# Optimization experiments

Measured on AMD Instinct MI355X. Metric: run time of the kernel, lower is better.

## Reference

```python
import jax, jax.numpy as jnp
import numpy as np

NS, NP, EJ, ER = 10000, 2048, 32768, 32768  # skills, job/resume pairs, edges
D, H = 1536, 8
NEG_SLOPE_ATT = 0.2   # GAT attention leaky_relu
NEG_SLOPE = 0.01      # F.leaky_relu / nn.LeakyReLU default


def setup_inputs() -> dict:
    key = jax.random.key(0)
    ks = jax.random.split(key, 20)
    rn = lambda k, shp, s=1.0: jax.random.normal(k, shp, dtype=jnp.float32) * s
    s_d = 1.0 / np.sqrt(D)
    return {
        "x_skill": rn(ks[0], (NS, D)),
        "x_job": rn(ks[1], (NP, D)),
        "x_resume": rn(ks[2], (NP, D)),
        # GraphConv params (lin_rel has bias, lin_root bias=False in PyG)
        "W_rel": rn(ks[3], (D, D), s_d),
        "b_rel": jnp.zeros((D,), jnp.float32),
        "W_root": rn(ks[4], (D, D), s_d),
        # GATConv params (heads=8, concat=False)
        "W_gat_src": rn(ks[5], (D, H * D), s_d),
        "W_gat_dst": rn(ks[6], (D, H * D), s_d),
        "att_src": rn(ks[7], (H, D), s_d),
        "att_dst": rn(ks[8], (H, D), s_d),
        "b_gat": jnp.zeros((D,), jnp.float32),
        # MLP: [3072 -> 512 -> 128 -> 1]
        "W1": rn(ks[9], (2 * D, 512), 1.0 / np.sqrt(2 * D)),
        "b1": jnp.zeros((512,), jnp.float32),
        "W2": rn(ks[10], (512, 128), 1.0 / np.sqrt(512)),
        "b2": jnp.zeros((128,), jnp.float32),
        "W3": rn(ks[11], (128, 1), 1.0 / np.sqrt(128)),
        "b3": jnp.zeros((1,), jnp.float32),
        # edge lists (src = skill idx, dst = job/resume idx)
        "edge_src_job": jax.random.randint(ks[12], (EJ,), 0, NS, dtype=jnp.int32),
        "edge_dst_job": jax.random.randint(ks[13], (EJ,), 0, NP, dtype=jnp.int32),
        "edge_src_res": jax.random.randint(ks[14], (ER,), 0, NS, dtype=jnp.int32),
        "edge_dst_res": jax.random.randint(ks[15], (ER,), 0, NP, dtype=jnp.int32),
    }


def reference(x_skill, x_job, x_resume, W_rel, b_rel, W_root,
              W_gat_src, W_gat_dst, att_src, att_dst, b_gat,
              W1, b1, W2, b2, W3, b3,
              edge_src_job, edge_dst_job, edge_src_res, edge_dst_res):
    n_pair = x_job.shape[0]

    # --- GraphConv (skill -> job): sum-aggregate then linear + root ---
    agg = jax.ops.segment_sum(x_skill[edge_src_job], edge_dst_job,
                              num_segments=n_pair)                  # [NP, D]
    h_job = agg @ W_rel + b_rel + x_job @ W_root                     # [NP, D]

    # --- GATConv (skill -> resume), heads=H, concat=False, no self-loops ---
    xs = (x_skill @ W_gat_src).reshape(-1, H, D)                     # [NS, H, D]
    xd = (x_resume @ W_gat_dst).reshape(-1, H, D)                    # [NP, H, D]
    a_src = jnp.einsum('nhd,hd->nh', xs, att_src)                    # [NS, H]
    a_dst = jnp.einsum('nhd,hd->nh', xd, att_dst)                    # [NP, H]
    e = jax.nn.leaky_relu(a_src[edge_src_res] + a_dst[edge_dst_res],
                          NEG_SLOPE_ATT)                             # [E, H]
    # segment softmax over edges grouped by destination resume node
    e_max = jax.ops.segment_max(e, edge_dst_res, num_segments=n_pair)
    e_exp = jnp.exp(e - e_max[edge_dst_res])
    denom = jax.ops.segment_sum(e_exp, edge_dst_res, num_segments=n_pair)
    alpha = e_exp / (denom[edge_dst_res] + 1e-16)                    # [E, H]
    msg = xs[edge_src_res] * alpha[:, :, None]                       # [E, H, D]
    out = jax.ops.segment_sum(msg, edge_dst_res, num_segments=n_pair)  # [NP, H, D]
    h_res = out.mean(axis=1) + b_gat                                 # concat=False -> head mean

    # --- combine + MLP ---
    h = jnp.concatenate([jax.nn.leaky_relu(h_job, NEG_SLOPE),
                         jax.nn.leaky_relu(h_res, NEG_SLOPE)], axis=1)  # [NP, 2D]
    h = jax.nn.leaky_relu(h @ W1 + b1, NEG_SLOPE)
    h = jax.nn.leaky_relu(h @ W2 + b2, NEG_SLOPE)
    score = (h @ W3 + b3).squeeze(-1)                                # [NP]
    return score, alpha
```

## Files before the change

kernel.cpp:

```cpp
#include <hip/hip_runtime.h>

#define D_ 1536
#define H_ 8

typedef __attribute__((ext_vector_type(8))) short bf16x8;
typedef __attribute__((ext_vector_type(4))) float f32x4;

__device__ __forceinline__ unsigned short f2bf(float f) {
    unsigned u = __builtin_bit_cast(unsigned, f);
    unsigned r = (u + 0x7fffu + ((u >> 16) & 1u)) >> 16;
    return (unsigned short)r;
}

__device__ __forceinline__ unsigned pack2bf(float a, float b) {
    return (unsigned)f2bf(a) | ((unsigned)f2bf(b) << 16);
}

__device__ __forceinline__ float bflo(unsigned u) { return __builtin_bit_cast(float, u << 16); }
__device__ __forceinline__ float bfhi(unsigned u) { return __builtin_bit_cast(float, u & 0xffff0000u); }

__device__ __forceinline__ void gload16(const void* g, void* l) {
    __builtin_amdgcn_global_load_lds((const __attribute__((address_space(1))) void*)g,
                                     (__attribute__((address_space(3))) void*)l, 16, 0, 0);
}

struct TrJob { const float* in; int ldin; unsigned short* out; int ldout; int nx; int gatb; };

__global__ __launch_bounds__(256) void k_prep(const float* __restrict__ W_gd,
                                              const float* __restrict__ att_d,
                                              float* __restrict__ Vdst,
                                              const float* __restrict__ W_gs,
                                              const float* __restrict__ att_s,
                                              float* __restrict__ Vsrc,
                                              unsigned short* __restrict__ BTg,
                                              const float* __restrict__ W_rel,
                                              const float* __restrict__ W_root,
                                              unsigned short* __restrict__ BT1,
                                              const float* __restrict__ W1,
                                              unsigned short* __restrict__ BTw1) {
    __shared__ float t[64][65];
    __shared__ float red[4][H_];
    int r = blockIdx.x;

    if (r < D_) {
        int d = r;
        const float4* wr = (const float4*)(W_gd + (size_t)d * (H_ * D_));
        int tid = threadIdx.x;
        float part[H_];
        #pragma unroll
        for (int h = 0; h < H_; h++) {
            const float4* ar = (const float4*)(att_d + h * D_);
            float4 w0 = wr[h * 384 + tid];
            float4 a0 = ar[tid];
            float s = w0.x * a0.x + w0.y * a0.y + w0.z * a0.z + w0.w * a0.w;
            if (tid < 128) {
                float4 w1 = wr[h * 384 + 256 + tid];
                float4 a1 = ar[256 + tid];
                s += w1.x * a1.x + w1.y * a1.y + w1.z * a1.z + w1.w * a1.w;
            }
            part[h] = s;
        }
        int lane = tid & 63, w = tid >> 6;
        #pragma unroll
        for (int h = 0; h < H_; h++) {
            float v = part[h];
            for (int o = 32; o; o >>= 1) v += __shfl_down(v, o);
            if (lane == 0) red[w][h] = v;
        }
        __syncthreads();
        if (tid < H_) Vdst[d * H_ + tid] = red[0][tid] + red[1][tid] + red[2][tid] + red[3][tid];
        return;
    }
    r -= D_;

    const float* in; int ldin; unsigned short* out; int ldout; int nx; int gatb;
    if (r < 4608)      { in = W_gs;  ldin = 0;    out = BTg;       ldout = H_ * D_; nx = 24; gatb = 1; }
    else if ((r -= 4608) < 576) { in = W_rel; ldin = D_;   out = BT1;       ldout = 2 * D_;  nx = 24; gatb = 0; }
    else if ((r -= 576) < 576)  { in = W_root;ldin = D_;   out = BT1 + D_;  ldout = 2 * D_;  nx = 24; gatb = 0; }
    else { r -= 576;              in = W1;    ldin = 512;  out = BTw1;      ldout = 2 * D_;  nx = 8;  gatb = 0; }

    int n0 = (r % nx) * 64, k0 = (r / nx) * 64;
    int tx = threadIdx.x & 63, ty = threadIdx.x >> 6;
    #pragma unroll
    for (int i = 0; i < 16; i++) {
        int k = k0 + ty + i * 4;
        const float* rp;
        if (gatb) {
            int d2 = k % D_, h = k / D_;
            rp = in + (size_t)d2 * (H_ * D_) + (size_t)h * D_;
        } else {
            rp = in + (size_t)k * ldin;
        }
        t[ty + i * 4][tx] = rp[n0 + tx];
    }
    __syncthreads();
    int tx2 = threadIdx.x & 31, ty2 = threadIdx.x >> 5;
    #pragma unroll
    for (int i = 0; i < 8; i++) {
        int nl = ty2 + i * 8;
        unsigned v = pack2bf(t[tx2 * 2][nl], t[tx2 * 2 + 1][nl]);
        *(unsigned*)(out + (size_t)(n0 + nl) * ldout + k0 + tx2 * 2) = v;
    }
    if (gatb) {
        int h = k0 / D_, d2b = k0 - h * D_;
        int kl = threadIdx.x >> 2, q = threadIdx.x & 3;
        const float* ar = att_s + (size_t)h * D_ + n0 + q * 16;
        float s = 0.f;
        #pragma unroll
        for (int i = 0; i < 16; i++) s += t[kl][q * 16 + i] * ar[i];
        s += __shfl_xor(s, 1);
        s += __shfl_xor(s, 2);
        if (q == 0) atomicAdd(&Vsrc[(size_t)(d2b + kl) * H_ + h], s);
    }
}

__global__ __launch_bounds__(256) void k_a2(const float* __restrict__ xs,
                                            const float* __restrict__ xr,
                                            const float* __restrict__ Vs,
                                            const float* __restrict__ Vd,
                                            float* __restrict__ a_s,
                                            float* __restrict__ a_d,
                                            unsigned* __restrict__ xb, int NS) {
    int n = blockIdx.x;
    int skill = n < NS;
    int row = skill ? n : n - NS;
    const float2* xrow = (const float2*)(skill ? xs : xr) + (size_t)row * 768;
    const float* V = skill ? Vs : Vd;
    float* out = (skill ? a_s : a_d) + (size_t)row * H_;
    unsigned* ob = xb + (size_t)row * 768;
    float part[H_] = {};
    #pragma unroll
    for (int j = 0; j < 3; j++) {
        int e = threadIdx.x + j * 256;
        float2 v = xrow[e];
        if (skill) ob[e] = pack2bf(v.x, v.y);
        const float* vp = V + (size_t)(2 * e) * H_;
        #pragma unroll
        for (int h = 0; h < H_; h++) part[h] += v.x * vp[h] + v.y * vp[h + H_];
    }
    __shared__ float red[4][H_];
    int lane = threadIdx.x & 63, w = threadIdx.x >> 6;
    #pragma unroll
    for (int h = 0; h < H_; h++) {
        float v = part[h];
        for (int o = 32; o; o >>= 1) v += __shfl_down(v, o);
        if (lane == 0) red[w][h] = v;
    }
    __syncthreads();
    if (threadIdx.x < H_) out[threadIdx.x] =
        red[0][threadIdx.x] + red[1][threadIdx.x] + red[2][threadIdx.x] + red[3][threadIdx.x];
}

__global__ void k_count(const int* __restrict__ dj, int ej, const int* __restrict__ dr, int er,
                        int* cnt_j, int* cnt_r) {
    int i = blockIdx.x * blockDim.x + threadIdx.x;
    if (i < ej) atomicAdd(&cnt_j[dj[i]], 1);
    else if (i < ej + er) atomicAdd(&cnt_r[dr[i - ej]], 1);
}

__global__ void k_scan(const int* __restrict__ cnt_j, int* off_j,
                       const int* __restrict__ cnt_r, int* off_r, int NP) {
    const int* cnt = blockIdx.x ? cnt_r : cnt_j;
    int* off = blockIdx.x ? off_r : off_j;
    int lane = threadIdx.x;
    int chunk = (NP + 63) / 64;
    int base = lane * chunk;
    int sum = 0;
    for (int i = 0; i < chunk; i++) { int idx = base + i; if (idx < NP) sum += cnt[idx]; }
    int incl = sum;
    for (int o = 1; o < 64; o <<= 1) { int t = __shfl_up(incl, o); if (lane >= o) incl += t; }
    int run = incl - sum;
    for (int i = 0; i < chunk; i++) { int idx = base + i; if (idx < NP) { off[idx] = run; run += cnt[idx]; } }
    if (lane == 63) off[NP] = run;
}

__global__ void k_scatter(const int* __restrict__ dj, const int* __restrict__ sj, int ej,
                          const int* __restrict__ dr, const int* __restrict__ sr, int er,
                          const int* __restrict__ off_j, int* fill_j, int* srcv_j,
                          const int* __restrict__ off_r, int* fill_r, int* sid_r, int* srcv_r) {
    int i = blockIdx.x * blockDim.x + threadIdx.x;
    if (i < ej) {
        int p = dj[i];
        int slot = atomicAdd(&fill_j[p], 1);
        srcv_j[off_j[p] + slot] = sj[i];
    } else if (i < ej + er) {
        int e = i - ej;
        int p = dr[e];
        int slot = atomicAdd(&fill_r[p], 1);
        int idx = off_r[p] + slot;
        sid_r[idx] = e;
        srcv_r[idx] = sr[e];
    }
}

__global__ void k_softmax(const float* __restrict__ a_src, const float* __restrict__ a_dst,
                          const int* __restrict__ srcv, const int* __restrict__ sid,
                          const int* __restrict__ cnt, const int* __restrict__ off,
                          float* __restrict__ alpha_out, float* __restrict__ alpha_s) {
    int p = blockIdx.x;
    int n = cnt[p], o = off[p];
    if (n == 0) return;
    int lane = threadIdx.x;
    float4 ad0 = *(const float4*)(a_dst + (size_t)p * H_);
    float4 ad1 = *(const float4*)(a_dst + (size_t)p * H_ + 4);
    float adv[8] = {ad0.x, ad0.y, ad0.z, ad0.w, ad1.x, ad1.y, ad1.z, ad1.w};
    if (n <= 64) {
        int e = 0;
        float v[8];
        if (lane < n) {
            e = sid[o + lane];
            int s = srcv[o + lane];
            float4 s0 = *(const float4*)(a_src + (size_t)s * H_);
            float4 s1 = *(const float4*)(a_src + (size_t)s * H_ + 4);
            float sv[8] = {s0.x, s0.y, s0.z, s0.w, s1.x, s1.y, s1.z, s1.w};
            #pragma unroll
            for (int h = 0; h < H_; h++) {
                float t = sv[h] + adv[h];
                v[h] = t >= 0.f ? t : 0.2f * t;
            }
        } else {
            #pragma unroll
            for (int h = 0; h < H_; h++) v[h] = -3.4e38f;
        }
        float ex[8];
        #pragma unroll
        for (int h = 0; h < H_; h++) {
            float m = v[h];
            for (int o2 = 32; o2; o2 >>= 1) m = fmaxf(m, __shfl_xor(m, o2));
            float ev = (lane < n) ? expf(v[h] - m) : 0.f;
            float s = ev;
            for (int o2 = 32; o2; o2 >>= 1) s += __shfl_xor(s, o2);
            ex[h] = ev / (s + 1e-16f);
        }
        if (lane < n) {
            *(float4*)(alpha_out + (size_t)e * H_) = make_float4(ex[0], ex[1], ex[2], ex[3]);
            *(float4*)(alpha_out + (size_t)e * H_ + 4) = make_float4(ex[4], ex[5], ex[6], ex[7]);
            *(float4*)(alpha_s + (size_t)(o + lane) * H_) = make_float4(ex[0], ex[1], ex[2], ex[3]);
            *(float4*)(alpha_s + (size_t)(o + lane) * H_ + 4) = make_float4(ex[4], ex[5], ex[6], ex[7]);
        }
    } else {
        #pragma unroll 1
        for (int h = 0; h < H_; h++) {
            float ad = adv[h];
            float m = -3.4e38f;
            for (int i = lane; i < n; i += 64) {
                float v = a_src[(size_t)srcv[o + i] * H_ + h] + ad;
                v = v >= 0.f ? v : 0.2f * v;
                m = fmaxf(m, v);
            }
            for (int o2 = 32; o2; o2 >>= 1) m = fmaxf(m, __shfl_xor(m, o2));
            float s = 0.f;
            for (int i = lane; i < n; i += 64) {
                float v = a_src[(size_t)srcv[o + i] * H_ + h] + ad;
                v = v >= 0.f ? v : 0.2f * v;
                s += expf(v - m);
            }
            for (int o2 = 32; o2; o2 >>= 1) s += __shfl_xor(s, o2);
            float inv = 1.f / (s + 1e-16f);
            for (int i = lane; i < n; i += 64) {
                float v = a_src[(size_t)srcv[o + i] * H_ + h] + ad;
                v = v >= 0.f ? v : 0.2f * v;
                float a = expf(v - m) * inv;
                alpha_out[(size_t)sid[o + i] * H_ + h] = a;
                alpha_s[(size_t)(o + i) * H_ + h] = a;
            }
        }
    }
}

__global__ __launch_bounds__(256) void k_aggs(const unsigned* __restrict__ xb,
                                              const int* __restrict__ srcv_j,
                                              const int* __restrict__ cnt_j, const int* __restrict__ off_j,
                                              const int* __restrict__ srcv_r,
                                              const int* __restrict__ cnt_r, const int* __restrict__ off_r,
                                              const float* __restrict__ alpha_s,
                                              const float* __restrict__ x_job,
                                              unsigned* __restrict__ cat_u,
                                              unsigned* __restrict__ aggatt_u) {
    int p = blockIdx.x;
    if (blockIdx.y < 3) {
        int col = blockIdx.y * 256 + threadIdx.x;
        int n = cnt_j[p], o = off_j[p];
        float2 acc = {0.f, 0.f};
        int i = 0;
        for (; i + 2 <= n; i += 2) {
            unsigned v0 = xb[(size_t)srcv_j[o + i] * 768 + col];
            unsigned v1 = xb[(size_t)srcv_j[o + i + 1] * 768 + col];
            acc.x += bflo(v0) + bflo(v1);
            acc.y += bfhi(v0) + bfhi(v1);
        }
        if (i < n) {
            unsigned v = xb[(size_t)srcv_j[o + i] * 768 + col];
            acc.x += bflo(v); acc.y += bfhi(v);
        }
        unsigned* orow = cat_u + (size_t)p * 1536;
        orow[col] = pack2bf(acc.x, acc.y);
        float2 vj = ((const float2*)x_job)[(size_t)p * 768 + col];
        orow[768 + col] = pack2bf(vj.x, vj.y);
    } else {
        int col = (blockIdx.y - 3) * 256 + threadIdx.x;
        int n = cnt_r[p], o = off_r[p];
        const float* as = alpha_s + (size_t)o * H_;
        float2 acc[H_] = {};
        int i = 0;
        for (; i + 2 <= n; i += 2) {
            unsigned v0 = xb[(size_t)srcv_r[o + i] * 768 + col];
            unsigned v1 = xb[(size_t)srcv_r[o + i + 1] * 768 + col];
            float l0 = bflo(v0), h0 = bfhi(v0), l1 = bflo(v1), h1 = bfhi(v1);
            const float* a0 = as + (size_t)i * H_;
            const float* a1 = a0 + H_;
            #pragma unroll
            for (int h = 0; h < H_; h++) {
                float w0 = a0[h], w1 = a1[h];
                acc[h].x += w0 * l0 + w1 * l1;
                acc[h].y += w0 * h0 + w1 * h1;
            }
        }
        if (i < n) {
            unsigned v0 = xb[(size_t)srcv_r[o + i] * 768 + col];
            float l0 = bflo(v0), h0 = bfhi(v0);
            const float* a0 = as + (size_t)i * H_;
            #pragma unroll
            for (int h = 0; h < H_; h++) { acc[h].x += a0[h] * l0; acc[h].y += a0[h] * h0; }
        }
        unsigned* orow = aggatt_u + (size_t)p * (H_ * 768);
        #pragma unroll
        for (int h = 0; h < H_; h++)
            orow[h * 768 + col] = pack2bf(acc[h].x, acc[h].y);
    }
}

__global__ __launch_bounds__(512, 4) void gemm_sk(const unsigned short* __restrict__ A, int lda,
                                                  const unsigned short* __restrict__ BT, int ldb,
                                                  float* __restrict__ P, int N, int bs, int extra) {
    __shared__ unsigned short As[3][256 * 32];
    __shared__ unsigned short Bs[3][128 * 32];
    int tid = threadIdx.x;
    int lane = tid & 63, wid = tid >> 6;

    int nwg = gridDim.x * gridDim.y;
    int bidh = blockIdx.y * gridDim.x + blockIdx.x;
    int swz = (bidh & 7) * (nwg >> 3) + (bidh >> 3);
    int bn = (swz % gridDim.x) * 128;
    int bm = (swz / gridDim.x) * 256;

    int z = blockIdx.z;
    int nt = bs + (z < extra);
    int kb = z * bs + min(z, extra);
    int kbase = kb * 32;

    int wr = wid >> 1, wc = wid & 1;
    int fr = lane & 15, g = lane >> 4;

    int ra0 = tid >> 2, sa0 = tid & 3;
    int ra1 = (tid + 512) >> 2;
    int sg_a0 = sa0 ^ ((ra0 >> 1) & 3);
    int sg_a1 = sa0 ^ ((ra1 >> 1) & 3);
    int sg_b = sg_a0;

    f32x4 acc[4][4] = {};

    auto stage = [&](int buf, int k0) {
        gload16(A + (size_t)(bm + ra0) * lda + k0 + sg_a0 * 8, &As[buf][tid * 8]);
        gload16(A + (size_t)(bm + ra1) * lda + k0 + sg_a1 * 8, &As[buf][(tid + 512) * 8]);
        gload16(BT + (size_t)(bn + ra0) * ldb + k0 + sg_b * 8, &Bs[buf][tid * 8]);
    };

    stage(0, kbase);
    if (nt > 1) stage(1, kbase + 32);
    for (int t = 0; t < nt; t++) {
        if (t + 2 < nt) {
            stage((t + 2) % 3, kbase + (t + 2) * 32);
            asm volatile("s_waitcnt vmcnt(6)" ::: "memory");
        } else if (t + 1 < nt) {
            asm volatile("s_waitcnt vmcnt(3)" ::: "memory");
        } else {
            asm volatile("s_waitcnt vmcnt(0)" ::: "memory");
        }
        __builtin_amdgcn_s_barrier();
        __builtin_amdgcn_sched_barrier(0);
        int cur = t % 3;
        bf16x8 a[4], b[4];
        #pragma unroll
        for (int mi = 0; mi < 4; mi++) {
            int row = wr * 64 + mi * 16 + fr;
            a[mi] = *(const bf16x8*)(&As[cur][row * 32 + ((g ^ ((row >> 1) & 3)) * 8)]);
        }
        #pragma unroll
        for (int ni = 0; ni < 4; ni++) {
            int row = wc * 64 + ni * 16 + fr;
            b[ni] = *(const bf16x8*)(&Bs[cur][row * 32 + ((g ^ ((row >> 1) & 3)) * 8)]);
        }
        __builtin_amdgcn_s_setprio(1);
        #pragma unroll
        for (int mi = 0; mi < 4; mi++)
            #pragma unroll
            for (int ni = 0; ni < 4; ni++)
                acc[mi][ni] = __builtin_amdgcn_mfma_f32_16x16x32_bf16(a[mi], b[ni], acc[mi][ni], 0, 0, 0);
        __builtin_amdgcn_s_setprio(0);
        __builtin_amdgcn_s_barrier();
        __builtin_amdgcn_sched_barrier(0);
    }

    size_t MN = (size_t)N * (size_t)(gridDim.y * 256);
    float* Pz = P + (size_t)z * MN;
    #pragma unroll
    for (int mi = 0; mi < 4; mi++) {
        int r0 = bm + wr * 64 + mi * 16 + (lane >> 4) * 4;
        #pragma unroll
        for (int ni = 0; ni < 4; ni++) {
            int c = bn + wc * 64 + ni * 16 + (lane & 15);
            #pragma unroll
            for (int j = 0; j < 4; j++)
                Pz[(size_t)(r0 + j) * N + c] = acc[mi][ni][j];
        }
    }
}

template <int OUT_BF16>
__global__ __launch_bounds__(256) void k_reduce(const float* __restrict__ P, int S, int MN, int N,
                                                void* __restrict__ Cout, int ldc,
                                                const float* __restrict__ bias, float scale,
                                                int useLeaky) {
    int idx = (blockIdx.x * 256 + threadIdx.x) * 4;
    if (idx >= MN) return;
    float4 v = *(const float4*)(P + idx);
    for (int s = 1; s < S; s++) {
        float4 t = *(const float4*)(P + (size_t)s * MN + idx);
        v.x += t.x; v.y += t.y; v.z += t.z; v.w += t.w;
    }
    int m = idx / N, n = idx - m * N;
    float vv[4] = {v.x, v.y, v.z, v.w};
    #pragma unroll
    for (int j = 0; j < 4; j++) {
        float x = vv[j] * scale + bias[n + j];
        if (useLeaky) x = x >= 0.f ? x : 0.01f * x;
        if (OUT_BF16) ((unsigned short*)Cout)[(size_t)m * ldc + n + j] = f2bf(x);
        else ((float*)Cout)[(size_t)m * ldc + n + j] = x;
    }
}

__global__ __launch_bounds__(256) void k_mlp2(const unsigned short* __restrict__ h1b,
                                              const float* __restrict__ W2,
                                              const float* __restrict__ b2,
                                              const float* __restrict__ W3,
                                              const float* __restrict__ b3,
                                              float* __restrict__ score) {
    __shared__ unsigned h1s[8][256];
    __shared__ float red[4][4];
    int p0 = blockIdx.x * 8;
    int tid = threadIdx.x;
    const unsigned* hsrc = (const unsigned*)h1b + (size_t)p0 * 256;
    #pragma unroll
    for (int i = 0; i < 8; i++) {
        int idx = tid + i * 256;
        h1s[idx >> 8][idx & 255] = hsrc[idx];
    }
    __syncthreads();
    int c = tid & 127, rg = tid >> 7;
    float acc[4] = {};
    for (int k = 0; k < 512; k += 2) {
        float w0 = W2[(size_t)k * 128 + c];
        float w1 = W2[(size_t)(k + 1) * 128 + c];
        #pragma unroll
        for (int r = 0; r < 4; r++) {
            unsigned hv = h1s[rg * 4 + r][k >> 1];
            acc[r] += bflo(hv) * w0 + bfhi(hv) * w1;
        }
    }
    float w3 = W3[c];
    float pr[4];
    #pragma unroll
    for (int r = 0; r < 4; r++) {
        float v = acc[r] + b2[c];
        v = v >= 0.f ? v : 0.01f * v;
        pr[r] = v * w3;
    }
    #pragma unroll
    for (int r = 0; r < 4; r++)
        for (int o = 32; o; o >>= 1) pr[r] += __shfl_down(pr[r], o);
    int w = tid >> 6;
    if ((tid & 63) == 0) {
        #pragma unroll
        for (int r = 0; r < 4; r++) red[w][r] = pr[r];
    }
    __syncthreads();
    if (tid < 8) {
        int rg2 = tid >> 2, r = tid & 3;
        float s = red[rg2 * 2][r] + red[rg2 * 2 + 1][r] + b3[0];
        score[p0 + rg2 * 4 + r] = s;
    }
}

extern "C" void kernel_launch(void* const* d_in, const int* in_sizes, int n_in,
                              void* d_out, int out_size, void* d_ws, size_t ws_size,
                              hipStream_t stream) {
    const float* x_skill = (const float*)d_in[0];
    const float* x_job   = (const float*)d_in[1];
    const float* x_resume= (const float*)d_in[2];
    const float* W_rel   = (const float*)d_in[3];
    const float* b_rel   = (const float*)d_in[4];
    const float* W_root  = (const float*)d_in[5];
    const float* W_gs    = (const float*)d_in[6];
    const float* W_gd    = (const float*)d_in[7];
    const float* att_s   = (const float*)d_in[8];
    const float* att_d   = (const float*)d_in[9];
    const float* b_gat   = (const float*)d_in[10];
    const float* W1      = (const float*)d_in[11];
    const float* b1      = (const float*)d_in[12];
    const float* W2      = (const float*)d_in[13];
    const float* b2      = (const float*)d_in[14];
    const float* W3      = (const float*)d_in[15];
    const float* b3      = (const float*)d_in[16];
    const int* esj = (const int*)d_in[17];
    const int* edj = (const int*)d_in[18];
    const int* esr = (const int*)d_in[19];
    const int* edr = (const int*)d_in[20];

    const int NS = in_sizes[0] / D_;
    const int NP = in_sizes[1] / D_;
    const int EJ = in_sizes[17];
    const int ER = in_sizes[19];

    float* score = (float*)d_out;
    float* alpha = score + NP;

    char* ws = (char*)d_ws;
    size_t off = 0;
    auto alloc = [&](size_t bytes) -> void* {
        void* p = ws + off;
        off = (off + bytes + 255) & ~(size_t)255;
        return p;
    };

    int* cnt_j  = (int*)alloc((size_t)4 * NP * sizeof(int));
    int* fill_j = cnt_j + NP;
    int* cnt_r  = cnt_j + 2 * NP;
    int* fill_r = cnt_j + 3 * NP;
    int* off_j  = (int*)alloc((size_t)(NP + 1) * sizeof(int));
    int* off_r  = (int*)alloc((size_t)(NP + 1) * sizeof(int));
    int* srcv_j = (int*)alloc((size_t)EJ * sizeof(int));
    int* sid_r  = (int*)alloc((size_t)ER * sizeof(int));
    int* srcv_r = (int*)alloc((size_t)ER * sizeof(int));
    float* alpha_s = (float*)alloc((size_t)ER * H_ * sizeof(float));
    float* Vsrc = (float*)alloc((size_t)D_ * H_ * 4);
    float* Vdst = (float*)alloc((size_t)D_ * H_ * 4);
    float* a_src= (float*)alloc((size_t)NS * H_ * 4);
    float* a_dst= (float*)alloc((size_t)NP * H_ * 4);
    unsigned short* cat_in = (unsigned short*)alloc((size_t)NP * 2 * D_ * 2);
    unsigned short* aggatt = (unsigned short*)alloc((size_t)NP * H_ * D_ * 2);
    unsigned short* BT1    = (unsigned short*)alloc((size_t)D_ * 2 * D_ * 2);
    unsigned short* BTg    = (unsigned short*)alloc((size_t)D_ * H_ * D_ * 2);
    unsigned short* BTw1   = (unsigned short*)alloc((size_t)512 * 2 * D_ * 2);
    unsigned short* hcat   = (unsigned short*)alloc((size_t)NP * 2 * D_ * 2);
    unsigned short* h1b    = (unsigned short*)alloc((size_t)NP * 512 * 2);
    float* Pbuf = (float*)alloc((size_t)5 * NP * D_ * 4);
    unsigned* xsb = (unsigned*)Pbuf;

    hipMemsetAsync(cnt_j, 0, (size_t)4 * NP * sizeof(int), stream);
    hipMemsetAsync(Vsrc, 0, (size_t)D_ * H_ * sizeof(float), stream);

    k_prep<<<D_ + 4608 + 576 + 576 + 384, 256, 0, stream>>>(
        W_gd, att_d, Vdst, W_gs, att_s, Vsrc, BTg, W_rel, W_root, BT1, W1, BTw1);

    k_a2<<<NS + NP, 256, 0, stream>>>(x_skill, x_resume, Vsrc, Vdst, a_src, a_dst, xsb, NS);

    int egrid = (EJ + ER + 255) / 256;
    k_count<<<egrid, 256, 0, stream>>>(edj, EJ, edr, ER, cnt_j, cnt_r);
    k_scan<<<2, 64, 0, stream>>>(cnt_j, off_j, cnt_r, off_r, NP);
    k_scatter<<<egrid, 256, 0, stream>>>(edj, esj, EJ, edr, esr, ER,
                                         off_j, fill_j, srcv_j,
                                         off_r, fill_r, sid_r, srcv_r);

    k_softmax<<<NP, 64, 0, stream>>>(a_src, a_dst, srcv_r, sid_r, cnt_r, off_r, alpha, alpha_s);
    k_aggs<<<dim3(NP, 6), 256, 0, stream>>>(xsb, srcv_j, cnt_j, off_j,
                                            srcv_r, cnt_r, off_r, alpha_s, x_job,
                                            (unsigned*)cat_in, (unsigned*)aggatt);

    const int MN_f = NP * D_;
    const int MN_1 = NP * 512;

    gemm_sk<<<dim3(D_ / 128, NP / 256, 5), 512, 0, stream>>>(
        cat_in, 2 * D_, BT1, 2 * D_, Pbuf, D_, 19, 1);
    k_reduce<1><<<MN_f / 1024, 256, 0, stream>>>(Pbuf, 5, MN_f, D_, hcat, 2 * D_, b_rel, 1.f, 1);

    gemm_sk<<<dim3(D_ / 128, NP / 256, 5), 512, 0, stream>>>(
        aggatt, H_ * D_, BTg, H_ * D_, Pbuf, D_, 76, 4);
    k_reduce<1><<<MN_f / 1024, 256, 0, stream>>>(Pbuf, 5, MN_f, D_, hcat + D_, 2 * D_, b_gat, 1.f / H_, 1);

    gemm_sk<<<dim3(512 / 128, NP / 256, 8), 512, 0, stream>>>(
        hcat, 2 * D_, BTw1, 2 * D_, Pbuf, 512, 12, 0);
    k_reduce<1><<<MN_1 / 1024, 256, 0, stream>>>(Pbuf, 8, MN_1, 512, h1b, 512, b1, 1.f, 1);

    k_mlp2<<<NP / 8, 256, 0, stream>>>(h1b, W2, b2, W3, b3, score);
}
```

Measured before the change: 392.2 us.

## Fuse edge count, scan, softmax and final reduce into neighbouring kernels

Edge-count blocks are folded into k_prep, and the two scan blocks are appended to k_a2. The segment softmax is recomputed inside each k_aggs resume block, with alphas held in shared memory, which removes the alpha_s round trip. The split-K reduce of the W1 GEMM plus its bias and leaky_relu moves into k_mlp2. This cuts four kernel launches and several intermediate buffers, but the softmax is now computed redundantly by three column blocks per node. The shared alpha buffer is fixed at 1024 edges per node and uses 32KB of shared memory, which may reduce occupancy.

```diff
diff --git a/kernel.cpp b/kernel.cpp
--- a/kernel.cpp
+++ b/kernel.cpp
@@ -23,8 +23,6 @@
     __builtin_amdgcn_global_load_lds((const __attribute__((address_space(1))) void*)g,
                                      (__attribute__((address_space(3))) void*)l, 16, 0, 0);
 }
-
-struct TrJob { const float* in; int ldin; unsigned short* out; int ldout; int nx; int gatb; };
 
 __global__ __launch_bounds__(256) void k_prep(const float* __restrict__ W_gd,
                                               const float* __restrict__ att_d,
@@ -37,7 +35,10 @@
                                               const float* __restrict__ W_root,
                                               unsigned short* __restrict__ BT1,
                                               const float* __restrict__ W1,
-                                              unsigned short* __restrict__ BTw1) {
+                                              unsigned short* __restrict__ BTw1,
+                                              const int* __restrict__ edj, int EJ,
+                                              const int* __restrict__ edr, int ER,
+                                              int* cnt_j, int* cnt_r) {
     __shared__ float t[64][65];
     __shared__ float red[4][H_];
     int r = blockIdx.x;
@@ -73,11 +74,18 @@
     }
     r -= D_;
 
+    if (r >= 6144) {
+        int i = (r - 6144) * 256 + threadIdx.x;
+        if (i < EJ) atomicAdd(&cnt_j[edj[i]], 1);
+        else if (i < EJ + ER) atomicAdd(&cnt_r[edr[i - EJ]], 1);
+        return;
+    }
+
     const float* in; int ldin; unsigned short* out; int ldout; int nx; int gatb;
-    if (r < 4608)      { in = W_gs;  ldin = 0;    out = BTg;       ldout = H_ * D_; nx = 24; gatb = 1; }
-    else if ((r -= 4608) < 576) { in = W_rel; ldin = D_;   out = BT1;       ldout = 2 * D_;  nx = 24; gatb = 0; }
-    else if ((r -= 576) < 576)  { in = W_root;ldin = D_;   out = BT1 + D_;  ldout = 2 * D_;  nx = 24; gatb = 0; }
-    else { r -= 576;              in = W1;    ldin = 512;  out = BTw1;      ldout = 2 * D_;  nx = 8;  gatb = 0; }
+    if (r < 4608)               { in = W_gs;  ldin = 0;   out = BTg;      ldout = H_ * D_; nx = 24; gatb = 1; }
+    else if ((r -= 4608) < 576) { in = W_rel; ldin = D_;  out = BT1;      ldout = 2 * D_;  nx = 24; gatb = 0; }
+    else if ((r -= 576) < 576)  { in = W_root;ldin = D_;  out = BT1 + D_; ldout = 2 * D_;  nx = 24; gatb = 0; }
+    else { r -= 576;              in = W1;    ldin = 512; out = BTw1;     ldout = 2 * D_;  nx = 8;  gatb = 0; }
 
     int n0 = (r % nx) * 64, k0 = (r / nx) * 64;
     int tx = threadIdx.x & 63, ty = threadIdx.x >> 6;
@@ -120,8 +128,27 @@
                                             const float* __restrict__ Vd,
                                             float* __restrict__ a_s,
                                             float* __restrict__ a_d,
-                                            unsigned* __restrict__ xb, int NS) {
+                                            unsigned* __restrict__ xb, int NS, int NPn,
+                                            const int* __restrict__ cnt_j, int* off_j,
+                                            const int* __restrict__ cnt_r, int* off_r) {
     int n = blockIdx.x;
+    if (n >= NS + NPn) {
+        if (threadIdx.x >= 64) return;
+        int which = n - NS - NPn;
+        const int* cnt = which ? cnt_r : cnt_j;
+        int* off = which ? off_r : off_j;
+        int lane = threadIdx.x;
+        int chunk = (NPn + 63) / 64;
+        int base = lane * chunk;
+        int sum = 0;
+        for (int i = 0; i < chunk; i++) { int idx = base + i; if (idx < NPn) sum += cnt[idx]; }
+        int incl = sum;
+        for (int o = 1; o < 64; o <<= 1) { int t = __shfl_up(incl, o); if (lane >= o) incl += t; }
+        int run = incl - sum;
+        for (int i = 0; i < chunk; i++) { int idx = base + i; if (idx < NPn) { off[idx] = run; run += cnt[idx]; } }
+        if (lane == 63) off[NPn] = run;
+        return;
+    }
     int skill = n < NS;
     int row = skill ? n : n - NS;
     const float2* xrow = (const float2*)(skill ? xs : xr) + (size_t)row * 768;
@@ -149,29 +176,6 @@
     __syncthreads();
     if (threadIdx.x < H_) out[threadIdx.x] =
         red[0][threadIdx.x] + red[1][threadIdx.x] + red[2][threadIdx.x] + red[3][threadIdx.x];
-}
-
-__global__ void k_count(const int* __restrict__ dj, int ej, const int* __restrict__ dr, int er,
-                        int* cnt_j, int* cnt_r) {
-    int i = blockIdx.x * blockDim.x + threadIdx.x;
-    if (i < ej) atomicAdd(&cnt_j[dj[i]], 1);
-    else if (i < ej + er) atomicAdd(&cnt_r[dr[i - ej]], 1);
-}
-
-__global__ void k_scan(const int* __restrict__ cnt_j, int* off_j,
-                       const int* __restrict__ cnt_r, int* off_r, int NP) {
-    const int* cnt = blockIdx.x ? cnt_r : cnt_j;
-    int* off = blockIdx.x ? off_r : off_j;
-    int lane = threadIdx.x;
-    int chunk = (NP + 63) / 64;
-    int base = lane * chunk;
-    int sum = 0;
-    for (int i = 0; i < chunk; i++) { int idx = base + i; if (idx < NP) sum += cnt[idx]; }
-    int incl = sum;
-    for (int o = 1; o < 64; o <<= 1) { int t = __shfl_up(incl, o); if (lane >= o) incl += t; }
-    int run = incl - sum;
-    for (int i = 0; i < chunk; i++) { int idx = base + i; if (idx < NP) { off[idx] = run; run += cnt[idx]; } }
-    if (lane == 63) off[NP] = run;
 }
 
 __global__ void k_scatter(const int* __restrict__ dj, const int* __restrict__ sj, int ej,
@@ -193,90 +197,18 @@
     }
 }
 
-__global__ void k_softmax(const float* __restrict__ a_src, const float* __restrict__ a_dst,
-                          const int* __restrict__ srcv, const int* __restrict__ sid,
-                          const int* __restrict__ cnt, const int* __restrict__ off,
-                          float* __restrict__ alpha_out, float* __restrict__ alpha_s) {
-    int p = blockIdx.x;
-    int n = cnt[p], o = off[p];
-    if (n == 0) return;
-    int lane = threadIdx.x;
-    float4 ad0 = *(const float4*)(a_dst + (size_t)p * H_);
-    float4 ad1 = *(const float4*)(a_dst + (size_t)p * H_ + 4);
-    float adv[8] = {ad0.x, ad0.y, ad0.z, ad0.w, ad1.x, ad1.y, ad1.z, ad1.w};
-    if (n <= 64) {
-        int e = 0;
-        float v[8];
-        if (lane < n) {
-            e = sid[o + lane];
-            int s = srcv[o + lane];
-            float4 s0 = *(const float4*)(a_src + (size_t)s * H_);
-            float4 s1 = *(const float4*)(a_src + (size_t)s * H_ + 4);
-            float sv[8] = {s0.x, s0.y, s0.z, s0.w, s1.x, s1.y, s1.z, s1.w};
-            #pragma unroll
-            for (int h = 0; h < H_; h++) {
-                float t = sv[h] + adv[h];
-                v[h] = t >= 0.f ? t : 0.2f * t;
-            }
-        } else {
-            #pragma unroll
-            for (int h = 0; h < H_; h++) v[h] = -3.4e38f;
-        }
-        float ex[8];
-        #pragma unroll
-        for (int h = 0; h < H_; h++) {
-            float m = v[h];
-            for (int o2 = 32; o2; o2 >>= 1) m = fmaxf(m, __shfl_xor(m, o2));
-            float ev = (lane < n) ? expf(v[h] - m) : 0.f;
-            float s = ev;
-            for (int o2 = 32; o2; o2 >>= 1) s += __shfl_xor(s, o2);
-            ex[h] = ev / (s + 1e-16f);
-        }
-        if (lane < n) {
-            *(float4*)(alpha_out + (size_t)e * H_) = make_float4(ex[0], ex[1], ex[2], ex[3]);
-            *(float4*)(alpha_out + (size_t)e * H_ + 4) = make_float4(ex[4], ex[5], ex[6], ex[7]);
-            *(float4*)(alpha_s + (size_t)(o + lane) * H_) = make_float4(ex[0], ex[1], ex[2], ex[3]);
-            *(float4*)(alpha_s + (size_t)(o + lane) * H_ + 4) = make_float4(ex[4], ex[5], ex[6], ex[7]);
-        }
-    } else {
-        #pragma unroll 1
-        for (int h = 0; h < H_; h++) {
-            float ad = adv[h];
-            float m = -3.4e38f;
-            for (int i = lane; i < n; i += 64) {
-                float v = a_src[(size_t)srcv[o + i] * H_ + h] + ad;
-                v = v >= 0.f ? v : 0.2f * v;
-                m = fmaxf(m, v);
-            }
-            for (int o2 = 32; o2; o2 >>= 1) m = fmaxf(m, __shfl_xor(m, o2));
-            float s = 0.f;
-            for (int i = lane; i < n; i += 64) {
-                float v = a_src[(size_t)srcv[o + i] * H_ + h] + ad;
-                v = v >= 0.f ? v : 0.2f * v;
-                s += expf(v - m);
-            }
-            for (int o2 = 32; o2; o2 >>= 1) s += __shfl_xor(s, o2);
-            float inv = 1.f / (s + 1e-16f);
-            for (int i = lane; i < n; i += 64) {
-                float v = a_src[(size_t)srcv[o + i] * H_ + h] + ad;
-                v = v >= 0.f ? v : 0.2f * v;
-                float a = expf(v - m) * inv;
-                alpha_out[(size_t)sid[o + i] * H_ + h] = a;
-                alpha_s[(size_t)(o + i) * H_ + h] = a;
-            }
-        }
-    }
-}
-
 __global__ __launch_bounds__(256) void k_aggs(const unsigned* __restrict__ xb,
                                               const int* __restrict__ srcv_j,
                                               const int* __restrict__ cnt_j, const int* __restrict__ off_j,
                                               const int* __restrict__ srcv_r,
+                                              const int* __restrict__ sid_r,
                                               const int* __restrict__ cnt_r, const int* __restrict__ off_r,
-                                              const float* __restrict__ alpha_s,
+                                              const float* __restrict__ a_src,
+                                              const float* __restrict__ a_dst,
                                               const float* __restrict__ x_job,
                                               unsigned* __restrict__ cat_u,
-                                              unsigned* __restrict__ aggatt_u) {
+                                              unsigned* __restrict__ aggatt_u,
+                                              float* __restrict__ alpha_out) {
     int p = blockIdx.x;
     if (blockIdx.y < 3) {
         int col = blockIdx.y * 256 + threadIdx.x;
@@ -297,37 +229,98 @@
         orow[col] = pack2bf(acc.x, acc.y);
         float2 vj = ((const float2*)x_job)[(size_t)p * 768 + col];
         orow[768 + col] = pack2bf(vj.x, vj.y);
-    } else {
-        int col = (blockIdx.y - 3) * 256 + threadIdx.x;
-        int n = cnt_r[p], o = off_r[p];
-        const float* as = alpha_s + (size_t)o * H_;
-        float2 acc[H_] = {};
-        int i = 0;
-        for (; i + 2 <= n; i += 2) {
-            unsigned v0 = xb[(size_t)srcv_r[o + i] * 768 + col];
-            unsigned v1 = xb[(size_t)srcv_r[o + i + 1] * 768 + col];
-            float l0 = bflo(v0), h0 = bfhi(v0), l1 = bflo(v1), h1 = bfhi(v1);
-            const float* a0 = as + (size_t)i * H_;
-            const float* a1 = a0 + H_;
-            #pragma unroll
-            for (int h = 0; h < H_; h++) {
-                float w0 = a0[h], w1 = a1[h];
-                acc[h].x += w0 * l0 + w1 * l1;
-                acc[h].y += w0 * h0 + w1 * h1;
+        return;
+    }
+
+    __shared__ float al[1024][H_];
+    int n = cnt_r[p], o = off_r[p];
+    int tid = threadIdx.x;
+
+    if (tid < 64 && n > 0) {
+        int lane = tid;
+        float4 ad0 = *(const float4*)(a_dst + (size_t)p * H_);
+        float4 ad1 = *(const float4*)(a_dst + (size_t)p * H_ + 4);
+        float adv[8] = {ad0.x, ad0.y, ad0.z, ad0.w, ad1.x, ad1.y, ad1.z, ad1.w};
+        float mx[8];
+        #pragma unroll
+        for (int h = 0; h < H_; h++) mx[h] = -3.4e38f;
+        for (int base = 0; base < n; base += 64) {
+            int i = base + lane;
+            if (i < n) {
+                int s = srcv_r[o + i];
+                float4 s0 = *(const float4*)(a_src + (size_t)s * H_);
+                float4 s1 = *(const float4*)(a_src + (size_t)s * H_ + 4);
+                float sv[8] = {s0.x, s0.y, s0.z, s0.w, s1.x, s1.y, s1.z, s1.w};
+                #pragma unroll
+                for (int h = 0; h < H_; h++) {
+                    float t = sv[h] + adv[h];
+                    t = t >= 0.f ? t : 0.2f * t;
+                    al[i][h] = t;
+                    mx[h] = fmaxf(mx[h], t);
+                }
             }
         }
-        if (i < n) {
-            unsigned v0 = xb[(size_t)srcv_r[o + i] * 768 + col];
-            float l0 = bflo(v0), h0 = bfhi(v0);
-            const float* a0 = as + (size_t)i * H_;
-            #pragma unroll
-            for (int h = 0; h < H_; h++) { acc[h].x += a0[h] * l0; acc[h].y += a0[h] * h0; }
-        }
-        unsigned* orow = aggatt_u + (size_t)p * (H_ * 768);
         #pragma unroll
         for (int h = 0; h < H_; h++)
-            orow[h * 768 + col] = pack2bf(acc[h].x, acc[h].y);
-    }
+            for (int o2 = 32; o2; o2 >>= 1) mx[h] = fmaxf(mx[h], __shfl_xor(mx[h], o2));
+        float sm[8] = {};
+        for (int base = 0; base < n; base += 64) {
+            int i = base + lane;
+            if (i < n) {
+                #pragma unroll
+                for (int h = 0; h < H_; h++) {
+                    float e = expf(al[i][h] - mx[h]);
+                    al[i][h] = e;
+                    sm[h] += e;
+                }
+            }
+        }
+        float inv[8];
+        #pragma unroll
+        for (int h = 0; h < H_; h++) {
+            for (int o2 = 32; o2; o2 >>= 1) sm[h] += __shfl_xor(sm[h], o2);
+            inv[h] = 1.f / (sm[h] + 1e-16f);
+        }
+        for (int base = 0; base < n; base += 64) {
+            int i = base + lane;
+            if (i < n) {
+                float a[8];
+                #pragma unroll
+                for (int h = 0; h < H_; h++) { a[h] = al[i][h] * inv[h]; al[i][h] = a[h]; }
+                if (blockIdx.y == 3) {
+                    int e = sid_r[o + i];
+                    *(float4*)(alpha_out + (size_t)e * H_) = make_float4(a[0], a[1], a[2], a[3]);
+                    *(float4*)(alpha_out + (size_t)e * H_ + 4) = make_float4(a[4], a[5], a[6], a[7]);
+                }
+            }
+        }
+    }
+    __syncthreads();
+
+    int col = (blockIdx.y - 3) * 256 + tid;
+    float2 acc[H_] = {};
+    int i = 0;
+    for (; i + 2 <= n; i += 2) {
+        unsigned v0 = xb[(size_t)srcv_r[o + i] * 768 + col];
+        unsigned v1 = xb[(size_t)srcv_r[o + i + 1] * 768 + col];
+        float l0 = bflo(v0), h0 = bfhi(v0), l1 = bflo(v1), h1 = bfhi(v1);
+        #pragma unroll
+        for (int h = 0; h < H_; h++) {
+            float w0 = al[i][h], w1 = al[i + 1][h];
+            acc[h].x += w0 * l0 + w1 * l1;
+            acc[h].y += w0 * h0 + w1 * h1;
+        }
+    }
+    if (i < n) {
+        unsigned v0 = xb[(size_t)srcv_r[o + i] * 768 + col];
+        float l0 = bflo(v0), h0 = bfhi(v0);
+        #pragma unroll
+        for (int h = 0; h < H_; h++) { acc[h].x += al[i][h] * l0; acc[h].y += al[i][h] * h0; }
+    }
+    unsigned* orow = aggatt_u + (size_t)p * (H_ * 768);
+    #pragma unroll
+    for (int h = 0; h < H_; h++)
+        orow[h * 768 + col] = pack2bf(acc[h].x, acc[h].y);
 }
 
 __global__ __launch_bounds__(512, 4) void gemm_sk(const unsigned short* __restrict__ A, int lda,
@@ -440,7 +433,8 @@
     }
 }
 
-__global__ __launch_bounds__(256) void k_mlp2(const unsigned short* __restrict__ h1b,
+__global__ __launch_bounds__(256) void k_mlp2(const float* __restrict__ P, int MN1,
+                                              const float* __restrict__ b1,
                                               const float* __restrict__ W2,
                                               const float* __restrict__ b2,
                                               const float* __restrict__ W3,
@@ -450,11 +444,22 @@
     __shared__ float red[4][4];
     int p0 = blockIdx.x * 8;
     int tid = threadIdx.x;
-    const unsigned* hsrc = (const unsigned*)h1b + (size_t)p0 * 256;
     #pragma unroll
     for (int i = 0; i < 8; i++) {
         int idx = tid + i * 256;
-        h1s[idx >> 8][idx & 255] = hsrc[idx];
+        int row = idx >> 8, c2 = idx & 255;
+        size_t base = (size_t)(p0 + row) * 512 + 2 * c2;
+        float2 v = {0.f, 0.f};
+        #pragma unroll
+        for (int s = 0; s < 8; s++) {
+            float2 t = *(const float2*)(P + (size_t)s * MN1 + base);
+            v.x += t.x; v.y += t.y;
+        }
+        float2 bb = *(const float2*)(b1 + 2 * c2);
+        v.x += bb.x; v.y += bb.y;
+        v.x = v.x >= 0.f ? v.x : 0.01f * v.x;
+        v.y = v.y >= 0.f ? v.y : 0.01f * v.y;
+        h1s[row][c2] = pack2bf(v.x, v.y);
     }
     __syncthreads();
     int c = tid & 127, rg = tid >> 7;
@@ -542,7 +547,6 @@
     int* srcv_j = (int*)alloc((size_t)EJ * sizeof(int));
     int* sid_r  = (int*)alloc((size_t)ER * sizeof(int));
     int* srcv_r = (int*)alloc((size_t)ER * sizeof(int));
-    float* alpha_s = (float*)alloc((size_t)ER * H_ * sizeof(float));
     float* Vsrc = (float*)alloc((size_t)D_ * H_ * 4);
     float* Vdst = (float*)alloc((size_t)D_ * H_ * 4);
     float* a_src= (float*)alloc((size_t)NS * H_ * 4);
@@ -553,29 +557,30 @@
     unsigned short* BTg    = (unsigned short*)alloc((size_t)D_ * H_ * D_ * 2);
     unsigned short* BTw1   = (unsigned short*)alloc((size_t)512 * 2 * D_ * 2);
     unsigned short* hcat   = (unsigned short*)alloc((size_t)NP * 2 * D_ * 2);
-    unsigned short* h1b    = (unsigned short*)alloc((size_t)NP * 512 * 2);
     float* Pbuf = (float*)alloc((size_t)5 * NP * D_ * 4);
     unsigned* xsb = (unsigned*)Pbuf;
 
     hipMemsetAsync(cnt_j, 0, (size_t)4 * NP * sizeof(int), stream);
     hipMemsetAsync(Vsrc, 0, (size_t)D_ * H_ * sizeof(float), stream);
 
-    k_prep<<<D_ + 4608 + 576 + 576 + 384, 256, 0, stream>>>(
-        W_gd, att_d, Vdst, W_gs, att_s, Vsrc, BTg, W_rel, W_root, BT1, W1, BTw1);
-
-    k_a2<<<NS + NP, 256, 0, stream>>>(x_skill, x_resume, Vsrc, Vdst, a_src, a_dst, xsb, NS);
-
     int egrid = (EJ + ER + 255) / 256;
-    k_count<<<egrid, 256, 0, stream>>>(edj, EJ, edr, ER, cnt_j, cnt_r);
-    k_scan<<<2, 64, 0, stream>>>(cnt_j, off_j, cnt_r, off_r, NP);
+    const int NPREP = D_ + 4608 + 576 + 576 + 384;
+
+    k_prep<<<NPREP + egrid, 256, 0, stream>>>(
+        W_gd, att_d, Vdst, W_gs, att_s, Vsrc, BTg, W_rel, W_root, BT1, W1, BTw1,
+        edj, EJ, edr, ER, cnt_j, cnt_r);
+
+    k_a2<<<NS + NP + 2, 256, 0, stream>>>(x_skill, x_resume, Vsrc, Vdst, a_src, a_dst, xsb,
+                                          NS, NP, cnt_j, off_j, cnt_r, off_r);
+
     k_scatter<<<egrid, 256, 0, stream>>>(edj, esj, EJ, edr, esr, ER,
                                          off_j, fill_j, srcv_j,
                                          off_r, fill_r, sid_r, srcv_r);
 
-    k_softmax<<<NP, 64, 0, stream>>>(a_src, a_dst, srcv_r, sid_r, cnt_r, off_r, alpha, alpha_s);
     k_aggs<<<dim3(NP, 6), 256, 0, stream>>>(xsb, srcv_j, cnt_j, off_j,
-                                            srcv_r, cnt_r, off_r, alpha_s, x_job,
-                                            (unsigned*)cat_in, (unsigned*)aggatt);
+                                            srcv_r, sid_r, cnt_r, off_r,
+                                            a_src, a_dst, x_job,
+                                            (unsigned*)cat_in, (unsigned*)aggatt, alpha);
 
     const int MN_f = NP * D_;
     const int MN_1 = NP * 512;
@@ -590,7 +595,6 @@
 
     gemm_sk<<<dim3(512 / 128, NP / 256, 8), 512, 0, stream>>>(
         hcat, 2 * D_, BTw1, 2 * D_, Pbuf, 512, 12, 0);
-    k_reduce<1><<<MN_1 / 1024, 256, 0, stream>>>(Pbuf, 8, MN_1, 512, h1b, 512, b1, 1.f, 1);
-
-    k_mlp2<<<NP / 8, 256, 0, stream>>>(h1b, W2, b2, W3, b3, score);
-}
+
+    k_mlp2<<<NP / 8, 256, 0, stream>>>(Pbuf, MN_1, b1, W2, b2, W3, b3, score);
+}
```

Result: slower. 403.3 us (+2.8%).
